# Optimization experiments

Measured on AMD Instinct MI355X. Metric: run time of the kernel, lower is better.

## Reference

```python
import jax, jax.numpy as jnp
import numpy as np

N_NODES = 50000
N_EDGES = 800000
IN_CH, HID_CH, OUT_CH = 128, 128, 64


def setup_inputs() -> dict:
    key = jax.random.key(0)
    k1, k2, k3, k4, k5, k6 = jax.random.split(key, 6)
    x = jax.random.normal(k1, (N_NODES, IN_CH), dtype=jnp.float32)
    edge_index = jax.random.randint(k2, (2, N_EDGES), 0, N_NODES, dtype=jnp.int64)
    # nn.Linear params: W [out, in], b [out]
    W1 = jax.random.normal(k3, (HID_CH, IN_CH), dtype=jnp.float32) / np.sqrt(IN_CH)
    b1 = jax.random.normal(k4, (HID_CH,), dtype=jnp.float32) * 0.01
    W2 = jax.random.normal(k5, (OUT_CH, HID_CH), dtype=jnp.float32) / np.sqrt(HID_CH)
    b2 = jax.random.normal(k6, (OUT_CH,), dtype=jnp.float32) * 0.01
    return {"x": x, "edge_index": edge_index, "W1": W1, "b1": b1, "W2": W2, "b2": b2}


def _aggregate(x, edge_index):
    # Faithful to SimpleGNN.aggregate: deg from ROW counts, normalization gathered at DST (col).
    row, col = edge_index[0], edge_index[1]
    n = x.shape[0]
    deg = jnp.bincount(row, length=n).astype(x.dtype)
    deg_inv = jnp.where(deg > 0, 1.0 / deg, 0.0)
    # out[dst] += x[src] * deg_inv[dst]  ==  segment_sum(x[src] by dst) * deg_inv[dst]
    agg = jax.ops.segment_sum(x[row], col, num_segments=n)
    return agg * deg_inv[:, None]


def reference(x, edge_index, W1, b1, W2, b2):
    h = x @ W1.T + b1                 # [N, hidden]
    h = _aggregate(h, edge_index)     # degree-normalized scatter-add
    out = h @ W2.T + b2               # [N, out]
    return out
```

## Files before the change

### kernel.cpp

```cpp
#include <hip/hip_runtime.h>
#include <hip/hip_bf16.h>


#define IN_CH   128
#define OUT_CH  64
#define NCHUNK  64
#define NRANGE  8
#define RBINS   6272
#define MC_PAD  40
#define YROWS   32
#define PLACE_BLOCKS (NCHUNK * NRANGE)
#define SMEM_FLOATS (IN_CH * OUT_CH + YROWS * (IN_CH + 4))

typedef unsigned short u16;
typedef unsigned int u32;

static __device__ inline float bfu32_lo(u32 u) { return __uint_as_float(u << 16); }
static __device__ inline float bfu32_hi(u32 u) { return __uint_as_float(u & 0xffff0000u); }
static __device__ inline u16 f2bf(float f) {
    __hip_bfloat16 h = __float2bfloat16(f);
    return *reinterpret_cast<u16*>(&h);
}

static __device__ inline int detect_stride_wave(const int* __restrict__ ei) {
    int lane = threadIdx.x & 63;
    int idx = (lane < 32) ? (2 * lane + 1) : 1;
    int v = ei[idx];
    unsigned long long m = __ballot((v != 0) && (lane < 32));
    return (m == 0ull) ? 2 : 1;
}

__global__ __launch_bounds__(256) void mk_prep(const float* __restrict__ W1,
                                               const float* __restrict__ b1,
                                               const float* __restrict__ W2,
                                               const int* __restrict__ ei,
                                               float* __restrict__ M,
                                               float* __restrict__ c,
                                               u16* __restrict__ row_slab,
                                               u16* __restrict__ col_slab,
                                               int n_edges, int n_nodes) {
    __shared__ u32 bins[RBINS];
    int b = blockIdx.x;
    int tid = threadIdx.x;
    if (b < MC_PAD) {
        int t = b * 256 + tid;
        if (t < IN_CH * OUT_CH) {
            int o = t & (OUT_CH - 1);
            int i = t >> 6;
            float acc = 0.f;
            for (int h = 0; h < 128; ++h)
                acc += W1[h * 128 + i] * W2[o * 128 + h];
            M[i * OUT_CH + o] = acc;
        } else if (t < IN_CH * OUT_CH + OUT_CH) {
            int o = t - IN_CH * OUT_CH;
            float acc = 0.f;
            for (int h = 0; h < 128; ++h)
                acc += b1[h] * W2[o * 128 + h];
            c[o] = acc;
        }
        return;
    }
    int hb = b - MC_PAD;
    int range = hb & (NRANGE - 1);
    int chunk = hb >> 3;

    int range_size = (n_nodes + NRANGE - 1) / NRANGE;
    int lo = range * range_size;
    int hi = lo + range_size; if (hi > n_nodes) hi = n_nodes;
    int nbins = hi - lo;
    if (nbins <= 0) return;

    int stride = detect_stride_wave(ei);
    for (int i = tid; i < nbins; i += 256) bins[i] = 0u;
    __syncthreads();

    size_t e0 = (size_t)chunk * n_edges / NCHUNK;
    size_t e1 = (size_t)(chunk + 1) * n_edges / NCHUNK;
    size_t cnt = e1 - e0;
    const int* rp = ei;
    const int* cp = ei + (size_t)n_edges * stride;

    size_t i = tid;
    int s[8], d[8];
    for (; i + 1792 < cnt; i += 2048) {
#pragma unroll
        for (int k = 0; k < 8; ++k) s[k] = rp[(e0 + i + 256 * k) * stride];
#pragma unroll
        for (int k = 0; k < 8; ++k) d[k] = cp[(e0 + i + 256 * k) * stride];
#pragma unroll
        for (int k = 0; k < 8; ++k) {
            if (s[k] >= lo && s[k] < hi) atomicAdd(&bins[s[k] - lo], 1u);
            if (d[k] >= lo && d[k] < hi && (unsigned)s[k] < (unsigned)n_nodes)
                atomicAdd(&bins[d[k] - lo], 0x10000u);
        }
    }
    for (; i < cnt; i += 256) {
        int ss = rp[(e0 + i) * stride];
        int dd = cp[(e0 + i) * stride];
        if (ss >= lo && ss < hi) atomicAdd(&bins[ss - lo], 1u);
        if (dd >= lo && dd < hi && (unsigned)ss < (unsigned)n_nodes)
            atomicAdd(&bins[dd - lo], 0x10000u);
    }
    __syncthreads();

    size_t base = (size_t)chunk * n_nodes + lo;
    for (int k = tid; k < nbins; k += 256) {
        u32 v = bins[k];
        row_slab[base + k] = (u16)(v & 0xFFFFu);
        col_slab[base + k] = (u16)(v >> 16);
    }
}

__global__ __launch_bounds__(256) void mk_choff(u16* __restrict__ row_slab,
                                                u16* __restrict__ col_slab,
                                                int* __restrict__ deg_row,
                                                int* __restrict__ cnt_col,
                                                int* __restrict__ cursor_part,
                                                int* __restrict__ bsums,
                                                int n_nodes) {
    __shared__ int sm[256];
    int t = threadIdx.x;
    int n = blockIdx.x * 256 + t;
    int run = 0;
    if (n < n_nodes) {
        int sum = 0;
#pragma unroll 8
        for (int ch = 0; ch < NCHUNK; ++ch)
            sum += row_slab[(size_t)ch * n_nodes + n];
        deg_row[n] = sum;
#pragma unroll 8
        for (int ch = 0; ch < NCHUNK; ++ch) {
            int v = col_slab[(size_t)ch * n_nodes + n];
            col_slab[(size_t)ch * n_nodes + n] = (u16)run;
            run += v;
        }
        cnt_col[n] = run;
    }
    sm[t] = run;
    __syncthreads();
    for (int d = 1; d < 256; d <<= 1) {
        int add = (t >= d) ? sm[t - d] : 0;
        __syncthreads();
        sm[t] += add;
        __syncthreads();
    }
    if (n < n_nodes) cursor_part[n] = sm[t] - run;
    if (t == 255) bsums[blockIdx.x] = sm[t];
}

static __device__ void block_bscan(const int* __restrict__ bsums, int nb,
                                   int* __restrict__ bscan) {
    int t = threadIdx.x;
    int v = (t < nb) ? bsums[t] : 0;
    bscan[t] = v;
    __syncthreads();
    for (int d = 1; d < 256; d <<= 1) {
        int add = (t >= d) ? bscan[t - d] : 0;
        __syncthreads();
        bscan[t] += add;
        __syncthreads();
    }
    bscan[t] -= v;
    __syncthreads();
}

__global__ __launch_bounds__(256) void mk_place_y(const int* __restrict__ ei,
                                                  const int* __restrict__ cursor_part,
                                                  const int* __restrict__ bsums,
                                                  const u16* __restrict__ col_slab,
                                                  int* __restrict__ csr_src,
                                                  const float* __restrict__ x,
                                                  const float* __restrict__ M,
                                                  u16* __restrict__ y,
                                                  int n_edges, int n_nodes, int nb) {
    __shared__ float smem[SMEM_FLOATS];
    int b = blockIdx.x;
    int tid = threadIdx.x;

    if (b < PLACE_BLOCKS) {
        int* rank = (int*)smem;
        int* bscan = (int*)smem + RBINS;
        block_bscan(bsums, nb, bscan);

        int range = b & (NRANGE - 1);
        int chunk = b >> 3;
        int range_size = (n_nodes + NRANGE - 1) / NRANGE;
        int lo = range * range_size;
        int hi = lo + range_size; if (hi > n_nodes) hi = n_nodes;
        if (hi <= lo) return;

        int stride = detect_stride_wave(ei);
        for (int i = tid; i < hi - lo; i += 256) rank[i] = 0;
        __syncthreads();

        size_t e0 = (size_t)chunk * n_edges / NCHUNK;
        size_t e1 = (size_t)(chunk + 1) * n_edges / NCHUNK;
        size_t cnt = e1 - e0;
        const int* rp = ei;
        const int* cp = ei + (size_t)n_edges * stride;
        size_t slab_base = (size_t)chunk * n_nodes;

        size_t i = tid;
        int s[8], d[8], cpart[8], coff[8];
        for (; i + 1792 < cnt; i += 2048) {
#pragma unroll
            for (int k = 0; k < 8; ++k) s[k] = rp[(e0 + i + 256 * k) * stride];
#pragma unroll
            for (int k = 0; k < 8; ++k) d[k] = cp[(e0 + i + 256 * k) * stride];
#pragma unroll
            for (int k = 0; k < 8; ++k) {
                int dc = (d[k] >= lo && d[k] < hi) ? d[k] : lo;
                cpart[k] = cursor_part[dc];
                coff[k]  = (int)col_slab[slab_base + dc];
            }
#pragma unroll
            for (int k = 0; k < 8; ++k) {
                if (d[k] >= lo && d[k] < hi && (unsigned)s[k] < (unsigned)n_nodes) {
                    int r = atomicAdd(&rank[d[k] - lo], 1);
                    csr_src[cpart[k] + bscan[d[k] >> 8] + coff[k] + r] = s[k];
                }
            }
        }
        for (; i < cnt; i += 256) {
            int ss = rp[(e0 + i) * stride];
            int dd = cp[(e0 + i) * stride];
            if (dd >= lo && dd < hi && (unsigned)ss < (unsigned)n_nodes) {
                int r = atomicAdd(&rank[dd - lo], 1);
                csr_src[cursor_part[dd] + bscan[dd >> 8] + (int)col_slab[slab_base + dd] + r] = ss;
            }
        }
        return;
    }

    int t = b - PLACE_BLOCKS;
    float* Ms = smem;
    float (*xs)[IN_CH + 4] = (float(*)[IN_CH + 4])(smem + IN_CH * OUT_CH);
    int tx = tid & 15;
    int ty = tid >> 4;
    int row0 = t * YROWS;
    if (row0 >= n_nodes) return;

    const float4* Mv = (const float4*)M;
    float4* Msv = (float4*)Ms;
#pragma unroll
    for (int k = 0; k < 8; ++k) Msv[tid + 256 * k] = Mv[tid + 256 * k];

    for (int f = tid; f < YROWS * 32; f += 256) {
        int r = f >> 5, kq = f & 31;
        float4 v = make_float4(0.f, 0.f, 0.f, 0.f);
        if (row0 + r < n_nodes)
            v = *(const float4*)&x[(size_t)(row0 + r) * IN_CH + 4 * kq];
        *(float4*)&xs[r][4 * kq] = v;
    }
    __syncthreads();

    float4 acc0 = make_float4(0.f, 0.f, 0.f, 0.f);
    float4 acc1 = make_float4(0.f, 0.f, 0.f, 0.f);

    for (int k = 0; k < IN_CH; k += 4) {
        float4 xr0 = *(const float4*)&xs[ty][k];
        float4 xr1 = *(const float4*)&xs[ty + 16][k];
        float4 m0 = *(const float4*)&Ms[(k + 0) * OUT_CH + 4 * tx];
        float4 m1 = *(const float4*)&Ms[(k + 1) * OUT_CH + 4 * tx];
        float4 m2 = *(const float4*)&Ms[(k + 2) * OUT_CH + 4 * tx];
        float4 m3 = *(const float4*)&Ms[(k + 3) * OUT_CH + 4 * tx];
        acc0.x = fmaf(xr0.x, m0.x, acc0.x); acc0.y = fmaf(xr0.x, m0.y, acc0.y);
        acc0.z = fmaf(xr0.x, m0.z, acc0.z); acc0.w = fmaf(xr0.x, m0.w, acc0.w);
        acc0.x = fmaf(xr0.y, m1.x, acc0.x); acc0.y = fmaf(xr0.y, m1.y, acc0.y);
        acc0.z = fmaf(xr0.y, m1.z, acc0.z); acc0.w = fmaf(xr0.y, m1.w, acc0.w);
        acc0.x = fmaf(xr0.z, m2.x, acc0.x); acc0.y = fmaf(xr0.z, m2.y, acc0.y);
        acc0.z = fmaf(xr0.z, m2.z, acc0.z); acc0.w = fmaf(xr0.z, m2.w, acc0.w);
        acc0.x = fmaf(xr0.w, m3.x, acc0.x); acc0.y = fmaf(xr0.w, m3.y, acc0.y);
        acc0.z = fmaf(xr0.w, m3.z, acc0.z); acc0.w = fmaf(xr0.w, m3.w, acc0.w);
        acc1.x = fmaf(xr1.x, m0.x, acc1.x); acc1.y = fmaf(xr1.x, m0.y, acc1.y);
        acc1.z = fmaf(xr1.x, m0.z, acc1.z); acc1.w = fmaf(xr1.x, m0.w, acc1.w);
        acc1.x = fmaf(xr1.y, m1.x, acc1.x); acc1.y = fmaf(xr1.y, m1.y, acc1.y);
        acc1.z = fmaf(xr1.y, m1.z, acc1.z); acc1.w = fmaf(xr1.y, m1.w, acc1.w);
        acc1.x = fmaf(xr1.z, m2.x, acc1.x); acc1.y = fmaf(xr1.z, m2.y, acc1.y);
        acc1.z = fmaf(xr1.z, m2.z, acc1.z); acc1.w = fmaf(xr1.z, m2.w, acc1.w);
        acc1.x = fmaf(xr1.w, m3.x, acc1.x); acc1.y = fmaf(xr1.w, m3.y, acc1.y);
        acc1.z = fmaf(xr1.w, m3.z, acc1.z); acc1.w = fmaf(xr1.w, m3.w, acc1.w);
    }

    int r0 = row0 + ty;
    int r1 = row0 + ty + 16;
    if (r0 < n_nodes) {
        ushort4 s4;
        s4.x = f2bf(acc0.x); s4.y = f2bf(acc0.y);
        s4.z = f2bf(acc0.z); s4.w = f2bf(acc0.w);
        *(ushort4*)&y[(size_t)r0 * OUT_CH + 4 * tx] = s4;
    }
    if (r1 < n_nodes) {
        ushort4 s4;
        s4.x = f2bf(acc1.x); s4.y = f2bf(acc1.y);
        s4.z = f2bf(acc1.z); s4.w = f2bf(acc1.w);
        *(ushort4*)&y[(size_t)r1 * OUT_CH + 4 * tx] = s4;
    }
}

__global__ __launch_bounds__(256) void mk_agg_final(const int* __restrict__ cursor_part,
                                                    const int* __restrict__ bsums,
                                                    const int* __restrict__ cnt_col,
                                                    const int* __restrict__ csr_src,
                                                    const int* __restrict__ deg_row,
                                                    const uint2* __restrict__ yv,
                                                    const float* __restrict__ c,
                                                    const float* __restrict__ b2,
                                                    float* __restrict__ out,
                                                    int n_nodes, int nb) {
    __shared__ int bscan[256];
    block_bscan(bsums, nb, bscan);

    int wave = threadIdx.x >> 6;
    int lane = threadIdx.x & 63;
    int dsub = lane >> 4;
    int ch   = lane & 15;
    int d = blockIdx.x * 16 + wave * 4 + dsub;
    if (d >= n_nodes) return;

    int start = cursor_part[d] + bscan[d >> 8];
    int cnt = cnt_col[d];
    int end = start + cnt;
    int e1m = end - 1;
    float a0 = 0.f, a1 = 0.f, a2 = 0.f, a3 = 0.f;

    if (cnt > 0) {
        int srcs[8];
#pragma unroll
        for (int k = 0; k < 8; ++k) {
            int t = start + k;
            srcs[k] = csr_src[t > e1m ? e1m : t];
        }
        for (int j = start; j < end; j += 8) {
            uint2 u[8];
#pragma unroll
            for (int k = 0; k < 8; ++k) u[k] = yv[(size_t)srcs[k] * 16 + ch];
            int nsrcs[8];
            int jn = j + 8;
#pragma unroll
            for (int k = 0; k < 8; ++k) {
                int t = jn + k;
                nsrcs[k] = csr_src[t > e1m ? e1m : t];
            }
#pragma unroll
            for (int k = 1; k < 8; ++k)
                if (j + k >= end) { u[k].x = 0u; u[k].y = 0u; }
#pragma unroll
            for (int k = 0; k < 8; ++k) {
                a0 += bfu32_lo(u[k].x);
                a1 += bfu32_hi(u[k].x);
                a2 += bfu32_lo(u[k].y);
                a3 += bfu32_hi(u[k].y);
            }
#pragma unroll
            for (int k = 0; k < 8; ++k) srcs[k] = nsrcs[k];
        }
    }

    int dr = deg_row[d];
    float di = (dr > 0) ? (1.0f / (float)dr) : 0.f;
    float fc = di * (float)cnt;
    float4 cv = ((const float4*)c)[ch];
    float4 bv = ((const float4*)b2)[ch];
    float4 o;
    o.x = di * a0 + fc * cv.x + bv.x;
    o.y = di * a1 + fc * cv.y + bv.y;
    o.z = di * a2 + fc * cv.z + bv.z;
    o.w = di * a3 + fc * cv.w + bv.w;
    ((float4*)(out + (size_t)d * OUT_CH))[ch] = o;
}

extern "C" void kernel_launch(void* const* d_in, const int* in_sizes, int n_in,
                              void* d_out, int out_size, void* d_ws, size_t ws_size,
                              hipStream_t stream) {
    const float* x  = (const float*)d_in[0];
    const int*   ei = (const int*)d_in[1];
    const float* W1 = (const float*)d_in[2];
    const float* b1 = (const float*)d_in[3];
    const float* W2 = (const float*)d_in[4];
    const float* b2 = (const float*)d_in[5];
    float* out = (float*)d_out;

    const int n_nodes = in_sizes[0] / IN_CH;
    const int n_edges = in_sizes[1] / 2;

    const size_t slab_bytes = (((size_t)NCHUNK * n_nodes * 2) + 127) & ~(size_t)127;
    const size_t csr_bytes  = ((size_t)n_edges * 4 + 127) & ~(size_t)127;

    char* ws = (char*)d_ws;
    float* M        = (float*)(ws);
    float* c        = (float*)(ws + 32768);
    int*   deg_row  = (int*)  (ws + 33152);
    int*   cnt_col  = (int*)  (ws + 233216);
    int*   cursor   = (int*)  (ws + 433280);
    int*   bsums    = (int*)  (ws + 633344);
    u16*   row_slab = (u16*)  (ws + 637440);
    u16*   col_slab = (u16*)  (ws + 637440 + slab_bytes);
    int*   csr_src  = (int*)  (ws + 637440 + 2 * slab_bytes);
    u16*   y        = (u16*)  (ws + 637440 + 2 * slab_bytes + csr_bytes);

    const int y_blocks = (n_nodes + YROWS - 1) / YROWS;
    const int nb = (n_nodes + 255) / 256;

    mk_prep<<<MC_PAD + NCHUNK * NRANGE, 256, 0, stream>>>(
        W1, b1, W2, ei, M, c, row_slab, col_slab, n_edges, n_nodes);

    mk_choff<<<nb, 256, 0, stream>>>(row_slab, col_slab, deg_row, cnt_col,
                                     cursor, bsums, n_nodes);

    mk_place_y<<<PLACE_BLOCKS + y_blocks, 256, 0, stream>>>(
        ei, cursor, bsums, col_slab, csr_src, x, M, y, n_edges, n_nodes, nb);

    mk_agg_final<<<(n_nodes + 15) / 16, 256, 0, stream>>>(
        cursor, bsums, cnt_col, csr_src, deg_row, (const uint2*)y, c, b2, out,
        n_nodes, nb);
}
```

Measured before the change: 155.4 us.

## Precompute per-node CSR base offsets in LDS and stage CSR segments in aggregation

In the placement kernel, each block now computes a per-node base offset (partition cursor + block scan + slab offset) once into shared memory. The edge loop then indexes csr_src with a single LDS lookup instead of two global gathers per edge. In the aggregation kernel, each block cooperatively loads its contiguous CSR source segment into LDS, so per-node index reads come from shared memory, and it falls back to global reads when the segment is too large. The cost is extra LDS use (which may lower occupancy), an added block barrier, and loss of the software-prefetch of next source indices.

Result: no change. 155.3 us (-0.1%).

```diff
diff --git a/kernel.cpp b/kernel.cpp
--- a/kernel.cpp
+++ b/kernel.cpp
@@ -10,7 +10,8 @@
 #define MC_PAD  40
 #define YROWS   32
 #define PLACE_BLOCKS (NCHUNK * NRANGE)
-#define SMEM_FLOATS (IN_CH * OUT_CH + YROWS * (IN_CH + 4))
+#define SMEM_BYTES 50176
+#define AGG_LDS 3072
 
 typedef unsigned short u16;
 typedef unsigned int u32;
@@ -173,14 +174,14 @@
                                                   const float* __restrict__ M,
                                                   u16* __restrict__ y,
                                                   int n_edges, int n_nodes, int nb) {
-    __shared__ float smem[SMEM_FLOATS];
+    __shared__ __align__(16) char smem_raw[SMEM_BYTES];
     int b = blockIdx.x;
     int tid = threadIdx.x;
 
     if (b < PLACE_BLOCKS) {
-        int* rank = (int*)smem;
-        int* bscan = (int*)smem + RBINS;
-        block_bscan(bsums, nb, bscan);
+        int* rank = (int*)smem_raw;
+        int* base = rank + RBINS;
+        block_bscan(bsums, nb, rank);
 
         int range = b & (NRANGE - 1);
         int chunk = b >> 3;
@@ -190,6 +191,11 @@
         if (hi <= lo) return;
 
         int stride = detect_stride_wave(ei);
+        size_t slab_base = (size_t)chunk * n_nodes;
+        for (int i = tid; i < hi - lo; i += 256)
+            base[i] = cursor_part[lo + i] + rank[(lo + i) >> 8]
+                    + (int)col_slab[slab_base + lo + i];
+        __syncthreads();
         for (int i = tid; i < hi - lo; i += 256) rank[i] = 0;
         __syncthreads();
 
@@ -198,26 +204,19 @@
         size_t cnt = e1 - e0;
         const int* rp = ei;
         const int* cp = ei + (size_t)n_edges * stride;
-        size_t slab_base = (size_t)chunk * n_nodes;
 
         size_t i = tid;
-        int s[8], d[8], cpart[8], coff[8];
+        int s[8], d[8];
         for (; i + 1792 < cnt; i += 2048) {
 #pragma unroll
             for (int k = 0; k < 8; ++k) s[k] = rp[(e0 + i + 256 * k) * stride];
 #pragma unroll
             for (int k = 0; k < 8; ++k) d[k] = cp[(e0 + i + 256 * k) * stride];
-#pragma unroll
-            for (int k = 0; k < 8; ++k) {
-                int dc = (d[k] >= lo && d[k] < hi) ? d[k] : lo;
-                cpart[k] = cursor_part[dc];
-                coff[k]  = (int)col_slab[slab_base + dc];
-            }
 #pragma unroll
             for (int k = 0; k < 8; ++k) {
                 if (d[k] >= lo && d[k] < hi && (unsigned)s[k] < (unsigned)n_nodes) {
                     int r = atomicAdd(&rank[d[k] - lo], 1);
-                    csr_src[cpart[k] + bscan[d[k] >> 8] + coff[k] + r] = s[k];
+                    csr_src[base[d[k] - lo] + r] = s[k];
                 }
             }
         }
@@ -226,15 +225,15 @@
             int dd = cp[(e0 + i) * stride];
             if (dd >= lo && dd < hi && (unsigned)ss < (unsigned)n_nodes) {
                 int r = atomicAdd(&rank[dd - lo], 1);
-                csr_src[cursor_part[dd] + bscan[dd >> 8] + (int)col_slab[slab_base + dd] + r] = ss;
+                csr_src[base[dd - lo] + r] = ss;
             }
         }
         return;
     }
 
     int t = b - PLACE_BLOCKS;
-    float* Ms = smem;
-    float (*xs)[IN_CH + 4] = (float(*)[IN_CH + 4])(smem + IN_CH * OUT_CH);
+    float* Ms = (float*)smem_raw;
+    float (*xs)[IN_CH + 4] = (float(*)[IN_CH + 4])((float*)smem_raw + IN_CH * OUT_CH);
     int tx = tid & 15;
     int ty = tid >> 4;
     int row0 = t * YROWS;
@@ -309,13 +308,27 @@
                                                     float* __restrict__ out,
                                                     int n_nodes, int nb) {
     __shared__ int bscan[256];
+    __shared__ int lcsr[AGG_LDS];
     block_bscan(bsums, nb, bscan);
 
-    int wave = threadIdx.x >> 6;
-    int lane = threadIdx.x & 63;
+    int tid = threadIdx.x;
+    int g = blockIdx.x;
+    int d0 = g * 16;
+    int dlast = d0 + 15; if (dlast > n_nodes - 1) dlast = n_nodes - 1;
+    int seg_base = cursor_part[d0] + bscan[d0 >> 8];
+    int seg_end  = cursor_part[dlast] + bscan[dlast >> 8] + cnt_col[dlast];
+    int seg_len  = seg_end - seg_base;
+    bool use_lds = (seg_len <= AGG_LDS);
+    if (use_lds) {
+        for (int i = tid; i < seg_len; i += 256) lcsr[i] = csr_src[seg_base + i];
+    }
+    __syncthreads();
+
+    int wave = tid >> 6;
+    int lane = tid & 63;
     int dsub = lane >> 4;
     int ch   = lane & 15;
-    int d = blockIdx.x * 16 + wave * 4 + dsub;
+    int d = d0 + wave * 4 + dsub;
     if (d >= n_nodes) return;
 
     int start = cursor_part[d] + bscan[d >> 8];
@@ -324,24 +337,17 @@
     int e1m = end - 1;
     float a0 = 0.f, a1 = 0.f, a2 = 0.f, a3 = 0.f;
 
-    if (cnt > 0) {
-        int srcs[8];
-#pragma unroll
-        for (int k = 0; k < 8; ++k) {
-            int t = start + k;
-            srcs[k] = csr_src[t > e1m ? e1m : t];
-        }
+    if (use_lds) {
         for (int j = start; j < end; j += 8) {
+            int srcs[8];
+#pragma unroll
+            for (int k = 0; k < 8; ++k) {
+                int t = j + k;
+                srcs[k] = lcsr[(t > e1m ? e1m : t) - seg_base];
+            }
             uint2 u[8];
 #pragma unroll
             for (int k = 0; k < 8; ++k) u[k] = yv[(size_t)srcs[k] * 16 + ch];
-            int nsrcs[8];
-            int jn = j + 8;
-#pragma unroll
-            for (int k = 0; k < 8; ++k) {
-                int t = jn + k;
-                nsrcs[k] = csr_src[t > e1m ? e1m : t];
-            }
 #pragma unroll
             for (int k = 1; k < 8; ++k)
                 if (j + k >= end) { u[k].x = 0u; u[k].y = 0u; }
@@ -352,8 +358,28 @@
                 a2 += bfu32_lo(u[k].y);
                 a3 += bfu32_hi(u[k].y);
             }
-#pragma unroll
-            for (int k = 0; k < 8; ++k) srcs[k] = nsrcs[k];
+        }
+    } else {
+        for (int j = start; j < end; j += 8) {
+            int srcs[8];
+#pragma unroll
+            for (int k = 0; k < 8; ++k) {
+                int t = j + k;
+                srcs[k] = csr_src[t > e1m ? e1m : t];
+            }
+            uint2 u[8];
+#pragma unroll
+            for (int k = 0; k < 8; ++k) u[k] = yv[(size_t)srcs[k] * 16 + ch];
+#pragma unroll
+            for (int k = 1; k < 8; ++k)
+                if (j + k >= end) { u[k].x = 0u; u[k].y = 0u; }
+#pragma unroll
+            for (int k = 0; k < 8; ++k) {
+                a0 += bfu32_lo(u[k].x);
+                a1 += bfu32_hi(u[k].x);
+                a2 += bfu32_lo(u[k].y);
+                a3 += bfu32_hi(u[k].y);
+            }
         }
     }
 
```
